# Kernel optimization log

Hardware: AMD Instinct MI355X
Metric: run time of the kernel (lower is better)

## Reference

```python
import jax, jax.numpy as jnp
import numpy as np

B = 262144
STATE_DIM = 12
ACTION_DIM = 1
MSG_DIM = 32
MAX_CHILDREN = 2
EPS = 1e-12  # F.normalize default eps


def _l2norm(x):
    n = jnp.sqrt(jnp.sum(x * x, axis=-1, keepdims=True))
    return x / jnp.maximum(n, EPS)


def setup_inputs() -> dict:
    key = jax.random.key(0)
    ks = jax.random.split(key, 16)

    def lin(kw, kb, out_d, in_d):
        lim = 1.0 / np.sqrt(in_d)
        w = jax.random.uniform(kw, (out_d, in_d), jnp.float32, -lim, lim)
        b = jax.random.uniform(kb, (out_d,), jnp.float32, -lim, lim)
        return w, b

    state = jax.random.normal(ks[0], (B, STATE_DIM), jnp.float32)
    action = jax.random.normal(ks[1], (B, ACTION_DIM), jnp.float32)

    # ModelUp (sNet): fc1, fc2, fc3
    up_w1, up_b1 = lin(ks[2], ks[3], 64, STATE_DIM + ACTION_DIM)
    up_w2, up_b2 = lin(ks[4], ks[5], 64, 64 + MSG_DIM * MAX_CHILDREN)
    up_w3, up_b3 = lin(ks[6], ks[7], MSG_DIM, 64)

    # ModelDownAction.model = MLPBase(msg_dim + action_dim + msg_dim, msg_dim)
    dyn_w1, dyn_b1 = lin(ks[8], ks[9], 400, MSG_DIM + ACTION_DIM + MSG_DIM)
    dyn_w2, dyn_b2 = lin(ks[10], ks[11], 300, 400)
    dyn_w3, dyn_b3 = lin(ks[12], ks[13], MSG_DIM, 300)

    return dict(state=state, action=action,
                up_w1=up_w1, up_b1=up_b1, up_w2=up_w2, up_b2=up_b2,
                up_w3=up_w3, up_b3=up_b3,
                dyn_w1=dyn_w1, dyn_b1=dyn_b1, dyn_w2=dyn_w2, dyn_b2=dyn_b2,
                dyn_w3=dyn_w3, dyn_b3=dyn_b3)


def reference(state, action,
              up_w1, up_b1, up_w2, up_b2, up_w3, up_b3,
              dyn_w1, dyn_b1, dyn_w2, dyn_b2, dyn_w3, dyn_b3):
    # num_limbs == 1, parents = [-1], td = bu = True, disable_fold = True
    x = state                              # (B, state_dim)
    u = action                             # (B, 1)

    # ---- bottom_up_transmission(0): ModelUp with all-zero child messages ----
    m_children = jnp.zeros((B, MSG_DIM * MAX_CHILDREN), x.dtype)
    xu = jnp.concatenate([x, u], axis=-1)
    xu = _l2norm(xu @ up_w1.T + up_b1)                       # (B, 64)
    xum = jnp.tanh(jnp.concatenate([xu, m_children], axis=-1))
    xum = jnp.tanh(xum @ up_w2.T + up_b2)                    # (B, 64)
    msg_up = _l2norm(xum @ up_w3.T + up_b3)                  # (B, msg_dim)

    # ---- top_down_transmission(0): ModelDownAction, state := msg_up ----
    # parent_msg = zeros, self_children_idx = 0 -> msg_in = zeros slice
    msg_in = jnp.zeros((B, MSG_DIM), x.dtype)
    xum2 = jnp.concatenate([msg_up, u, msg_in], axis=-1)     # (B, 2*msg_dim+1)
    h = jax.nn.relu(xum2 @ dyn_w1.T + dyn_b1)                # (B, 400)
    h = jax.nn.relu(h @ dyn_w2.T + dyn_b2)                   # (B, 300)
    delta = h @ dyn_w3.T + dyn_b3                            # (B, msg_dim)

    # stack over num_limbs=1 then squeeze -> (B, msg_dim)
    return delta
```

## Files before the change

### kernel.cpp

```cpp
#include <hip/hip_runtime.h>
#include <stdint.h>

typedef short s16x8 __attribute__((ext_vector_type(8)));
typedef float f32x16 __attribute__((ext_vector_type(16)));
typedef unsigned int u32;
typedef unsigned int u32x2 __attribute__((ext_vector_type(2)));

#define NFRAG 336
#define WS_USHORTS (NFRAG*512)
#define PANEL_BYTES 28672
#define LDS_BYTES (2*PANEL_BYTES)

#define MFMA(a,b,c) __builtin_amdgcn_mfma_f32_32x32x16_bf16((a),(b),(c),0,0,0)

__device__ __forceinline__ unsigned short f2bf(float f){
  u32 x = __builtin_bit_cast(u32, f);
  x += 0x7fffu + ((x >> 16) & 1u);
  return (unsigned short)(x >> 16);
}

__device__ __forceinline__ float bfhi(float b){
  return __builtin_bit_cast(float, (u32)f2bf(b) << 16);
}

__device__ __forceinline__ u32 pkbf(float a, float b){
  u32 r;
  asm("v_cvt_pk_bf16_f32 %0, %1, %2" : "=v"(r) : "v"(a), "v"(b));
  return r;
}

__device__ __forceinline__ float fast_tanh(float x){
  float ax = fabsf(x);
  float e = __expf(-2.0f * ax);
  float r = (1.0f - e) * __builtin_amdgcn_rcpf(1.0f + e);
  return x < 0.0f ? -r : r;
}

__device__ __forceinline__ float halfsum(float s){
  return s + __shfl_xor(s, 32);
}

__device__ __forceinline__ void tile2frags(const f32x16 v, s16x8& f0, s16x8& f1){
  u32 w00 = pkbf(v[0],  v[1]),  w01 = pkbf(v[2],  v[3]);
  u32 w10 = pkbf(v[4],  v[5]),  w11 = pkbf(v[6],  v[7]);
  u32 w20 = pkbf(v[8],  v[9]),  w21 = pkbf(v[10], v[11]);
  u32 w30 = pkbf(v[12], v[13]), w31 = pkbf(v[14], v[15]);
  u32x2 p0 = __builtin_amdgcn_permlane32_swap(w00, w10, false, false);
  u32x2 p1 = __builtin_amdgcn_permlane32_swap(w01, w11, false, false);
  u32x2 p2 = __builtin_amdgcn_permlane32_swap(w20, w30, false, false);
  u32x2 p3 = __builtin_amdgcn_permlane32_swap(w21, w31, false, false);
  int4 r0, r1;
  r0.x = (int)p0[0]; r0.y = (int)p1[0]; r0.z = (int)p0[1]; r0.w = (int)p1[1];
  r1.x = (int)p2[0]; r1.y = (int)p3[0]; r1.z = (int)p2[1]; r1.w = (int)p3[1];
  f0 = __builtin_bit_cast(s16x8, r0);
  f1 = __builtin_bit_cast(s16x8, r1);
}

__global__ void wconv_kernel(const float* __restrict__ uw1, const float* __restrict__ ub1,
                             const float* __restrict__ uw2, const float* __restrict__ ub2,
                             const float* __restrict__ uw3, const float* __restrict__ ub3,
                             const float* __restrict__ dw1, const float* __restrict__ db1,
                             const float* __restrict__ dw2, const float* __restrict__ db2,
                             const float* __restrict__ dw3, const float* __restrict__ db3,
                             unsigned short* __restrict__ wp)
{
  int i = blockIdx.x*256 + threadIdx.x;
  if (i >= WS_USHORTS) return;
  int f    = i >> 9;
  int lane = (i >> 3) & 63;
  int j    = i & 7;
  int row  = lane & 31;
  int k8   = (lane >> 5)*8 + j;
  float v = 0.0f;
  if (f < 2){
    int feat = f*32 + row; int k = k8;
    if (k < 13) v = uw1[feat*13 + k];
    else if (k == 13) v = ub1[feat];
    else if (k == 14) v = ub1[feat] - bfhi(ub1[feat]);
  } else if (f < 12){
    int t = f - 2; int kt = t >> 1, nt = t & 1;
    int feat = nt*32 + row; int k = kt*16 + k8;
    if (k < 64) v = uw2[feat*128 + k];
    else if (k == 64) v = ub2[feat];
    else if (k == 65) v = ub2[feat] - bfhi(ub2[feat]);
  } else if (f < 17){
    int kt = f - 12; int feat = row; int k = kt*16 + k8;
    if (k < 64) v = uw3[feat*64 + k];
    else if (k == 64) v = ub3[feat];
    else if (k == 65) v = ub3[feat] - bfhi(ub3[feat]);
  } else if (f < 56){
    int t = f - 17; int nt = t/3, kt = t%3;
    int feat = nt*32 + row; int k = kt*16 + k8;
    if (feat < 400){
      if (k < 33) v = dw1[feat*65 + k];
      else if (k == 33) v = db1[feat];
      else if (k == 34) v = db1[feat] - bfhi(db1[feat]);
    } else if ((feat == 400 || feat == 401) && k == 33) v = 1.0f;
  } else {
    int t = f - 56; int n = t/56; int r = t%56;
    if (r < 52){
      int kf = r >> 1, nt = r & 1;
      int feat = n*64 + nt*32 + row; int k = kf*16 + k8;
      if (feat < 300){
        if (k < 400) v = dw2[feat*400 + k];
        else if (k == 400) v = db2[feat];
        else if (k == 401) v = db2[feat] - bfhi(db2[feat]);
      } else if ((feat == 300 || feat == 301) && k == 400) v = 1.0f;
    } else {
      int kt = n*4 + (r - 52); int feat = row; int k = kt*16 + k8;
      if (k < 300) v = dw3[feat*300 + k];
      else if (k == 300) v = db3[feat];
      else if (k == 301) v = db3[feat] - bfhi(db3[feat]);
    }
  }
  wp[i] = f2bf(v);
}

__device__ __forceinline__ s16x8 frag_at(const char* P, int idx, int ln){
  return *(const s16x8*)(P + idx*1024 + ln*16);
}

__device__ __forceinline__ void stage_chunk(const unsigned short* wp, char* dst,
                                            int fbase, int nf, int tid){
  const char* src = (const char*)wp + (size_t)fbase*1024;
  int nbytes = nf*1024;
  #pragma unroll
  for (int j = 0; j < 7; ++j){
    int off = j*4096 + tid*16;
    if (off < nbytes)
      __builtin_amdgcn_global_load_lds(
        (const __attribute__((address_space(1))) unsigned int*)(src + off),
        (__attribute__((address_space(3))) unsigned int*)(dst + off), 16, 0, 0);
  }
}

__global__ __launch_bounds__(256, 2) void fused_kernel(
    const float* __restrict__ state, const float* __restrict__ action,
    const unsigned short* __restrict__ wp, float* __restrict__ out)
{
  __shared__ __align__(1024) char sm[LDS_BYTES];
  char* B0 = sm;
  char* B1 = sm + PANEL_BYTES;

  const int tid = threadIdx.x;
  const int ln  = tid & 63;
  const int wid = tid >> 6;
  const int c   = ln & 31;
  const int h   = ln >> 5;
  const int rowb = blockIdx.x*128 + wid*32;

  const float* xr = state + (size_t)(rowb + c)*12;
  float u = action[rowb + c];
  float4 xa, xb;
  if (h == 0){
    xa = *(const float4*)xr;
    xb = *(const float4*)(xr + 4);
  } else {
    xa = *(const float4*)(xr + 8);
    xb = float4{u, 1.0f, 1.0f, 0.0f};
  }

  stage_chunk(wp, B0, 0, 17, tid);
  __syncthreads();
  stage_chunk(wp, B1, 17, 21, tid);

  int4 xw;
  xw.x = pkbf(xa.x, xa.y); xw.y = pkbf(xa.z, xa.w);
  xw.z = pkbf(xb.x, xb.y); xw.w = pkbf(xb.z, xb.w);
  s16x8 xfrag = __builtin_bit_cast(s16x8, xw);
  int4 ow = {0,0,0,0}; if (h == 0) ow.x = 0x3F803F80;
  s16x8 onef = __builtin_bit_cast(s16x8, ow);
  int4 mw = {0,0,0,0};
  if (h == 0){ mw.x = pkbf(u, 1.0f); mw.y = 0x3F80; }
  s16x8 mf2 = __builtin_bit_cast(s16x8, mw);

  s16x8 mf0, mf1;
  {
    s16x8 xf0, xf1, xf2, xf3, tf0, tf1, tf2, tf3;
    {
      f32x16 a0 = {}, a1 = {};
      a0 = MFMA(frag_at(B0, 0, ln), xfrag, a0);
      a1 = MFMA(frag_at(B0, 1, ln), xfrag, a1);
      float s = 0.f;
      #pragma unroll
      for (int r = 0; r < 16; ++r) s += a0[r]*a0[r] + a1[r]*a1[r];
      s = halfsum(s);
      float inv = __builtin_amdgcn_rsqf(fmaxf(s, 1e-24f));
      #pragma unroll
      for (int r = 0; r < 16; ++r){
        a0[r] = fast_tanh(a0[r]*inv);
        a1[r] = fast_tanh(a1[r]*inv);
      }
      tile2frags(a0, xf0, xf1);
      tile2frags(a1, xf2, xf3);
    }
    {
      f32x16 a0 = {}, a1 = {};
      __builtin_amdgcn_s_setprio(1);
      a0 = MFMA(frag_at(B0, 2, ln), xf0, a0);  a1 = MFMA(frag_at(B0, 3, ln), xf0, a1);
      a0 = MFMA(frag_at(B0, 4, ln), xf1, a0);  a1 = MFMA(frag_at(B0, 5, ln), xf1, a1);
      a0 = MFMA(frag_at(B0, 6, ln), xf2, a0);  a1 = MFMA(frag_at(B0, 7, ln), xf2, a1);
      a0 = MFMA(frag_at(B0, 8, ln), xf3, a0);  a1 = MFMA(frag_at(B0, 9, ln), xf3, a1);
      a0 = MFMA(frag_at(B0,10, ln), onef, a0); a1 = MFMA(frag_at(B0,11, ln), onef, a1);
      __builtin_amdgcn_s_setprio(0);
      #pragma unroll
      for (int r = 0; r < 16; ++r){
        a0[r] = fast_tanh(a0[r]);
        a1[r] = fast_tanh(a1[r]);
      }
      tile2frags(a0, tf0, tf1);
      tile2frags(a1, tf2, tf3);
    }
    {
      f32x16 m = {};
      __builtin_amdgcn_s_setprio(1);
      m = MFMA(frag_at(B0,12, ln), tf0, m);
      m = MFMA(frag_at(B0,13, ln), tf1, m);
      m = MFMA(frag_at(B0,14, ln), tf2, m);
      m = MFMA(frag_at(B0,15, ln), tf3, m);
      m = MFMA(frag_at(B0,16, ln), onef, m);
      __builtin_amdgcn_s_setprio(0);
      float s = 0.f;
      #pragma unroll
      for (int r = 0; r < 16; ++r) s += m[r]*m[r];
      s = halfsum(s);
      float inv = __builtin_amdgcn_rsqf(fmaxf(s, 1e-24f));
      #pragma unroll
      for (int r = 0; r < 16; ++r) m[r] *= inv;
      tile2frags(m, mf0, mf1);
    }
  }

  s16x8 h1f[26];

  __syncthreads();
  stage_chunk(wp, B0, 38, 18, tid);
  #pragma unroll
  for (int nt = 0; nt < 7; ++nt){
    f32x16 a = {};
    __builtin_amdgcn_s_setprio(1);
    a = MFMA(frag_at(B1, nt*3+0, ln), mf0, a);
    a = MFMA(frag_at(B1, nt*3+1, ln), mf1, a);
    a = MFMA(frag_at(B1, nt*3+2, ln), mf2, a);
    __builtin_amdgcn_s_setprio(0);
    #pragma unroll
    for (int r = 0; r < 16; ++r) a[r] = fmaxf(a[r], 0.f);
    tile2frags(a, h1f[2*nt], h1f[2*nt+1]);
  }

  __syncthreads();
  stage_chunk(wp, B1, 56, 28, tid);
  #pragma unroll
  for (int nt = 0; nt < 6; ++nt){
    f32x16 a = {};
    __builtin_amdgcn_s_setprio(1);
    a = MFMA(frag_at(B0, nt*3+0, ln), mf0, a);
    a = MFMA(frag_at(B0, nt*3+1, ln), mf1, a);
    a = MFMA(frag_at(B0, nt*3+2, ln), mf2, a);
    __builtin_amdgcn_s_setprio(0);
    #pragma unroll
    for (int r = 0; r < 16; ++r) a[r] = fmaxf(a[r], 0.f);
    tile2frags(a, h1f[14 + 2*nt], h1f[14 + 2*nt+1]);
  }

  f32x16 acc3 = {};
  #pragma unroll 1
  for (int n = 0; n < 5; ++n){
    f32x16 d2a0 = {}, d2a1 = {};

    __syncthreads();
    stage_chunk(wp, B0, 84 + 56*n, 28, tid);
    __builtin_amdgcn_s_setprio(1);
    #pragma unroll
    for (int kfl = 0; kfl < 14; ++kfl){
      s16x8 hb = h1f[kfl];
      d2a0 = MFMA(frag_at(B1, kfl*2+0, ln), hb, d2a0);
      d2a1 = MFMA(frag_at(B1, kfl*2+1, ln), hb, d2a1);
    }
    __builtin_amdgcn_s_setprio(0);

    __syncthreads();
    if (n < 4) stage_chunk(wp, B1, 56 + 56*(n+1), 28, tid);
    __builtin_amdgcn_s_setprio(1);
    #pragma unroll
    for (int kfl = 0; kfl < 12; ++kfl){
      s16x8 hb = h1f[14 + kfl];
      d2a0 = MFMA(frag_at(B0, kfl*2+0, ln), hb, d2a0);
      d2a1 = MFMA(frag_at(B0, kfl*2+1, ln), hb, d2a1);
    }
    __builtin_amdgcn_s_setprio(0);
    #pragma unroll
    for (int r = 0; r < 16; ++r){
      d2a0[r] = fmaxf(d2a0[r], 0.f);
      d2a1[r] = fmaxf(d2a1[r], 0.f);
    }
    s16x8 c0, c1, c2, c3;
    tile2frags(d2a0, c0, c1);
    tile2frags(d2a1, c2, c3);
    __builtin_amdgcn_s_setprio(1);
    acc3 = MFMA(frag_at(B0, 24, ln), c0, acc3);
    acc3 = MFMA(frag_at(B0, 25, ln), c1, acc3);
    acc3 = MFMA(frag_at(B0, 26, ln), c2, acc3);
    acc3 = MFMA(frag_at(B0, 27, ln), c3, acc3);
    __builtin_amdgcn_s_setprio(0);
  }

  float* op = out + (size_t)(rowb + c)*32;
  #pragma unroll
  for (int p = 0; p < 4; ++p){
    float4 v4 = {acc3[4*p+0], acc3[4*p+1], acc3[4*p+2], acc3[4*p+3]};
    *(float4*)(op + p*8 + h*4) = v4;
  }
}

extern "C" void kernel_launch(void* const* d_in, const int* in_sizes, int n_in,
                              void* d_out, int out_size, void* d_ws, size_t ws_size,
                              hipStream_t stream)
{
  const float* state  = (const float*)d_in[0];
  const float* action = (const float*)d_in[1];
  const float* up_w1  = (const float*)d_in[2];
  const float* up_b1  = (const float*)d_in[3];
  const float* up_w2  = (const float*)d_in[4];
  const float* up_b2  = (const float*)d_in[5];
  const float* up_w3  = (const float*)d_in[6];
  const float* up_b3  = (const float*)d_in[7];
  const float* dyn_w1 = (const float*)d_in[8];
  const float* dyn_b1 = (const float*)d_in[9];
  const float* dyn_w2 = (const float*)d_in[10];
  const float* dyn_b2 = (const float*)d_in[11];
  const float* dyn_w3 = (const float*)d_in[12];
  const float* dyn_b3 = (const float*)d_in[13];
  unsigned short* wp = (unsigned short*)d_ws;

  hipLaunchKernelGGL(wconv_kernel, dim3((WS_USHORTS + 255)/256), dim3(256), 0, stream,
                     up_w1, up_b1, up_w2, up_b2, up_w3, up_b3,
                     dyn_w1, dyn_b1, dyn_w2, dyn_b2, dyn_w3, dyn_b3, wp);
  hipLaunchKernelGGL(fused_kernel, dim3(262144/128), dim3(256), 0, stream,
                     state, action, wp, (float*)d_out);
}
```

Measured before the change: 95.67 us.

## Stream weights in uniform 16-fragment panels with smaller 2-wave blocks

Replaces the irregular chunk staging (17/21/18/28-fragment chunks in two 28KB panels) with a uniform ring of 16KB panels, each holding 16 weight fragments, and addresses fragments by a global index. Panel loads are issued at fixed barrier points spread through the layer computations, so the double buffer advances at a steady rate. Blocks shrink from 4 waves/128 rows to 2 waves/64 rows, halving LDS per block so more blocks fit per CU. The cost is that each block stages the full weight set for half as many rows, doubling total global-to-LDS weight traffic, and there are more barriers.

```diff
diff --git a/kernel.cpp b/kernel.cpp
--- a/kernel.cpp
+++ b/kernel.cpp
@@ -8,7 +8,7 @@
 
 #define NFRAG 336
 #define WS_USHORTS (NFRAG*512)
-#define PANEL_BYTES 28672
+#define PANEL_BYTES 16384
 #define LDS_BYTES (2*PANEL_BYTES)
 
 #define MFMA(a,b,c) __builtin_amdgcn_mfma_f32_32x32x16_bf16((a),(b),(c),0,0,0)
@@ -116,38 +116,73 @@
   wp[i] = f2bf(v);
 }
 
-__device__ __forceinline__ s16x8 frag_at(const char* P, int idx, int ln){
-  return *(const s16x8*)(P + idx*1024 + ln*16);
-}
-
-__device__ __forceinline__ void stage_chunk(const unsigned short* wp, char* dst,
-                                            int fbase, int nf, int tid){
-  const char* src = (const char*)wp + (size_t)fbase*1024;
-  int nbytes = nf*1024;
+__device__ __forceinline__ s16x8 fragF(const char* sm, int f, int ln){
+  return *(const s16x8*)(sm + ((f >> 4) & 1)*PANEL_BYTES + (f & 15)*1024 + ln*16);
+}
+
+__device__ __forceinline__ void stage16(const unsigned short* wp, char* sm, int panel, int tid){
+  char* dst = sm + (panel & 1)*PANEL_BYTES;
+  const char* src = (const char*)wp + (size_t)panel*PANEL_BYTES;
   #pragma unroll
-  for (int j = 0; j < 7; ++j){
-    int off = j*4096 + tid*16;
-    if (off < nbytes)
-      __builtin_amdgcn_global_load_lds(
-        (const __attribute__((address_space(1))) unsigned int*)(src + off),
-        (__attribute__((address_space(3))) unsigned int*)(dst + off), 16, 0, 0);
-  }
-}
-
-__global__ __launch_bounds__(256, 2) void fused_kernel(
+  for (int j = 0; j < 8; ++j){
+    int off = j*2048 + tid*16;
+    __builtin_amdgcn_global_load_lds(
+      (const __attribute__((address_space(1))) unsigned int*)(src + off),
+      (__attribute__((address_space(3))) unsigned int*)(dst + off), 16, 0, 0);
+  }
+}
+
+#define BND(P) { __syncthreads(); if ((P) <= 20) stage16(wp, sm, (P), tid); }
+
+#define D1TRIPLE(f0_, oA, oB) { \
+  f32x16 a = {}; \
+  __builtin_amdgcn_s_setprio(1); \
+  a = MFMA(fragF(sm, (f0_)+0, ln), mf0, a); \
+  a = MFMA(fragF(sm, (f0_)+1, ln), mf1, a); \
+  a = MFMA(fragF(sm, (f0_)+2, ln), mf2, a); \
+  __builtin_amdgcn_s_setprio(0); \
+  _Pragma("unroll") \
+  for (int r = 0; r < 16; ++r) a[r] = fmaxf(a[r], 0.f); \
+  tile2frags(a, oA, oB); }
+
+#define D2RUN(fb, r0, r1) { \
+  __builtin_amdgcn_s_setprio(1); \
+  _Pragma("unroll") \
+  for (int r = (r0); r < (r1); ++r){ \
+    s16x8 hb = h1f[r>>1]; \
+    if (r & 1) d2a1 = MFMA(fragF(sm, (fb)+r, ln), hb, d2a1); \
+    else       d2a0 = MFMA(fragF(sm, (fb)+r, ln), hb, d2a0); \
+  } \
+  __builtin_amdgcn_s_setprio(0); }
+
+#define D2TAIL(fb) { \
+  _Pragma("unroll") \
+  for (int r = 0; r < 16; ++r){ \
+    d2a0[r] = fmaxf(d2a0[r], 0.f); \
+    d2a1[r] = fmaxf(d2a1[r], 0.f); \
+  } \
+  s16x8 c0, c1, c2, c3; \
+  tile2frags(d2a0, c0, c1); \
+  tile2frags(d2a1, c2, c3); \
+  __builtin_amdgcn_s_setprio(1); \
+  acc3 = MFMA(fragF(sm, (fb)+52, ln), c0, acc3); \
+  acc3 = MFMA(fragF(sm, (fb)+53, ln), c1, acc3); \
+  acc3 = MFMA(fragF(sm, (fb)+54, ln), c2, acc3); \
+  acc3 = MFMA(fragF(sm, (fb)+55, ln), c3, acc3); \
+  __builtin_amdgcn_s_setprio(0); }
+
+__global__ __launch_bounds__(128, 2) void fused_kernel(
     const float* __restrict__ state, const float* __restrict__ action,
     const unsigned short* __restrict__ wp, float* __restrict__ out)
 {
   __shared__ __align__(1024) char sm[LDS_BYTES];
-  char* B0 = sm;
-  char* B1 = sm + PANEL_BYTES;
 
   const int tid = threadIdx.x;
   const int ln  = tid & 63;
   const int wid = tid >> 6;
   const int c   = ln & 31;
   const int h   = ln >> 5;
-  const int rowb = blockIdx.x*128 + wid*32;
+  const int rowb = blockIdx.x*64 + wid*32;
 
   const float* xr = state + (size_t)(rowb + c)*12;
   float u = action[rowb + c];
@@ -160,9 +195,8 @@
     xb = float4{u, 1.0f, 1.0f, 0.0f};
   }
 
-  stage_chunk(wp, B0, 0, 17, tid);
-  __syncthreads();
-  stage_chunk(wp, B1, 17, 21, tid);
+  stage16(wp, sm, 0, tid);
+  BND(1)
 
   int4 xw;
   xw.x = pkbf(xa.x, xa.y); xw.y = pkbf(xa.z, xa.w);
@@ -179,8 +213,8 @@
     s16x8 xf0, xf1, xf2, xf3, tf0, tf1, tf2, tf3;
     {
       f32x16 a0 = {}, a1 = {};
-      a0 = MFMA(frag_at(B0, 0, ln), xfrag, a0);
-      a1 = MFMA(frag_at(B0, 1, ln), xfrag, a1);
+      a0 = MFMA(fragF(sm, 0, ln), xfrag, a0);
+      a1 = MFMA(fragF(sm, 1, ln), xfrag, a1);
       float s = 0.f;
       #pragma unroll
       for (int r = 0; r < 16; ++r) s += a0[r]*a0[r] + a1[r]*a1[r];
@@ -197,11 +231,11 @@
     {
       f32x16 a0 = {}, a1 = {};
       __builtin_amdgcn_s_setprio(1);
-      a0 = MFMA(frag_at(B0, 2, ln), xf0, a0);  a1 = MFMA(frag_at(B0, 3, ln), xf0, a1);
-      a0 = MFMA(frag_at(B0, 4, ln), xf1, a0);  a1 = MFMA(frag_at(B0, 5, ln), xf1, a1);
-      a0 = MFMA(frag_at(B0, 6, ln), xf2, a0);  a1 = MFMA(frag_at(B0, 7, ln), xf2, a1);
-      a0 = MFMA(frag_at(B0, 8, ln), xf3, a0);  a1 = MFMA(frag_at(B0, 9, ln), xf3, a1);
-      a0 = MFMA(frag_at(B0,10, ln), onef, a0); a1 = MFMA(frag_at(B0,11, ln), onef, a1);
+      a0 = MFMA(fragF(sm, 2, ln), xf0, a0);  a1 = MFMA(fragF(sm, 3, ln), xf0, a1);
+      a0 = MFMA(fragF(sm, 4, ln), xf1, a0);  a1 = MFMA(fragF(sm, 5, ln), xf1, a1);
+      a0 = MFMA(fragF(sm, 6, ln), xf2, a0);  a1 = MFMA(fragF(sm, 7, ln), xf2, a1);
+      a0 = MFMA(fragF(sm, 8, ln), xf3, a0);  a1 = MFMA(fragF(sm, 9, ln), xf3, a1);
+      a0 = MFMA(fragF(sm,10, ln), onef, a0); a1 = MFMA(fragF(sm,11, ln), onef, a1);
       __builtin_amdgcn_s_setprio(0);
       #pragma unroll
       for (int r = 0; r < 16; ++r){
@@ -214,11 +248,14 @@
     {
       f32x16 m = {};
       __builtin_amdgcn_s_setprio(1);
-      m = MFMA(frag_at(B0,12, ln), tf0, m);
-      m = MFMA(frag_at(B0,13, ln), tf1, m);
-      m = MFMA(frag_at(B0,14, ln), tf2, m);
-      m = MFMA(frag_at(B0,15, ln), tf3, m);
-      m = MFMA(frag_at(B0,16, ln), onef, m);
+      m = MFMA(fragF(sm,12, ln), tf0, m);
+      m = MFMA(fragF(sm,13, ln), tf1, m);
+      m = MFMA(fragF(sm,14, ln), tf2, m);
+      m = MFMA(fragF(sm,15, ln), tf3, m);
+      __builtin_amdgcn_s_setprio(0);
+      BND(2)
+      __builtin_amdgcn_s_setprio(1);
+      m = MFMA(fragF(sm,16, ln), onef, m);
       __builtin_amdgcn_s_setprio(0);
       float s = 0.f;
       #pragma unroll
@@ -232,77 +269,91 @@
   }
 
   s16x8 h1f[26];
-
-  __syncthreads();
-  stage_chunk(wp, B0, 38, 18, tid);
-  #pragma unroll
-  for (int nt = 0; nt < 7; ++nt){
+  D1TRIPLE(17, h1f[0],  h1f[1])
+  D1TRIPLE(20, h1f[2],  h1f[3])
+  D1TRIPLE(23, h1f[4],  h1f[5])
+  D1TRIPLE(26, h1f[6],  h1f[7])
+  D1TRIPLE(29, h1f[8],  h1f[9])
+  BND(3)
+  D1TRIPLE(32, h1f[10], h1f[11])
+  D1TRIPLE(35, h1f[12], h1f[13])
+  D1TRIPLE(38, h1f[14], h1f[15])
+  D1TRIPLE(41, h1f[16], h1f[17])
+  D1TRIPLE(44, h1f[18], h1f[19])
+  {
     f32x16 a = {};
     __builtin_amdgcn_s_setprio(1);
-    a = MFMA(frag_at(B1, nt*3+0, ln), mf0, a);
-    a = MFMA(frag_at(B1, nt*3+1, ln), mf1, a);
-    a = MFMA(frag_at(B1, nt*3+2, ln), mf2, a);
+    a = MFMA(fragF(sm, 47, ln), mf0, a);
+    __builtin_amdgcn_s_setprio(0);
+    BND(4)
+    __builtin_amdgcn_s_setprio(1);
+    a = MFMA(fragF(sm, 48, ln), mf1, a);
+    a = MFMA(fragF(sm, 49, ln), mf2, a);
     __builtin_amdgcn_s_setprio(0);
     #pragma unroll
     for (int r = 0; r < 16; ++r) a[r] = fmaxf(a[r], 0.f);
-    tile2frags(a, h1f[2*nt], h1f[2*nt+1]);
-  }
-
-  __syncthreads();
-  stage_chunk(wp, B1, 56, 28, tid);
-  #pragma unroll
-  for (int nt = 0; nt < 6; ++nt){
-    f32x16 a = {};
-    __builtin_amdgcn_s_setprio(1);
-    a = MFMA(frag_at(B0, nt*3+0, ln), mf0, a);
-    a = MFMA(frag_at(B0, nt*3+1, ln), mf1, a);
-    a = MFMA(frag_at(B0, nt*3+2, ln), mf2, a);
-    __builtin_amdgcn_s_setprio(0);
-    #pragma unroll
-    for (int r = 0; r < 16; ++r) a[r] = fmaxf(a[r], 0.f);
-    tile2frags(a, h1f[14 + 2*nt], h1f[14 + 2*nt+1]);
-  }
+    tile2frags(a, h1f[20], h1f[21]);
+  }
+  D1TRIPLE(50, h1f[22], h1f[23])
+  D1TRIPLE(53, h1f[24], h1f[25])
 
   f32x16 acc3 = {};
-  #pragma unroll 1
-  for (int n = 0; n < 5; ++n){
-    f32x16 d2a0 = {}, d2a1 = {};
-
-    __syncthreads();
-    stage_chunk(wp, B0, 84 + 56*n, 28, tid);
-    __builtin_amdgcn_s_setprio(1);
-    #pragma unroll
-    for (int kfl = 0; kfl < 14; ++kfl){
-      s16x8 hb = h1f[kfl];
-      d2a0 = MFMA(frag_at(B1, kfl*2+0, ln), hb, d2a0);
-      d2a1 = MFMA(frag_at(B1, kfl*2+1, ln), hb, d2a1);
-    }
-    __builtin_amdgcn_s_setprio(0);
-
-    __syncthreads();
-    if (n < 4) stage_chunk(wp, B1, 56 + 56*(n+1), 28, tid);
-    __builtin_amdgcn_s_setprio(1);
-    #pragma unroll
-    for (int kfl = 0; kfl < 12; ++kfl){
-      s16x8 hb = h1f[14 + kfl];
-      d2a0 = MFMA(frag_at(B0, kfl*2+0, ln), hb, d2a0);
-      d2a1 = MFMA(frag_at(B0, kfl*2+1, ln), hb, d2a1);
-    }
-    __builtin_amdgcn_s_setprio(0);
-    #pragma unroll
-    for (int r = 0; r < 16; ++r){
-      d2a0[r] = fmaxf(d2a0[r], 0.f);
-      d2a1[r] = fmaxf(d2a1[r], 0.f);
-    }
-    s16x8 c0, c1, c2, c3;
-    tile2frags(d2a0, c0, c1);
-    tile2frags(d2a1, c2, c3);
-    __builtin_amdgcn_s_setprio(1);
-    acc3 = MFMA(frag_at(B0, 24, ln), c0, acc3);
-    acc3 = MFMA(frag_at(B0, 25, ln), c1, acc3);
-    acc3 = MFMA(frag_at(B0, 26, ln), c2, acc3);
-    acc3 = MFMA(frag_at(B0, 27, ln), c3, acc3);
-    __builtin_amdgcn_s_setprio(0);
+  {
+    f32x16 d2a0 = {}, d2a1 = {};
+    D2RUN(56, 0, 8)
+    BND(5)
+    D2RUN(56, 8, 24)
+    BND(6)
+    D2RUN(56, 24, 40)
+    BND(7)
+    D2RUN(56, 40, 52)
+    D2TAIL(56)
+  }
+  {
+    f32x16 d2a0 = {}, d2a1 = {};
+    BND(8)
+    D2RUN(112, 0, 16)
+    BND(9)
+    D2RUN(112, 16, 32)
+    BND(10)
+    D2RUN(112, 32, 48)
+    BND(11)
+    D2RUN(112, 48, 52)
+    D2TAIL(112)
+  }
+  {
+    f32x16 d2a0 = {}, d2a1 = {};
+    D2RUN(168, 0, 8)
+    BND(12)
+    D2RUN(168, 8, 24)
+    BND(13)
+    D2RUN(168, 24, 40)
+    BND(14)
+    D2RUN(168, 40, 52)
+    D2TAIL(168)
+  }
+  {
+    f32x16 d2a0 = {}, d2a1 = {};
+    BND(15)
+    D2RUN(224, 0, 16)
+    BND(16)
+    D2RUN(224, 16, 32)
+    BND(17)
+    D2RUN(224, 32, 48)
+    BND(18)
+    D2RUN(224, 48, 52)
+    D2TAIL(224)
+  }
+  {
+    f32x16 d2a0 = {}, d2a1 = {};
+    D2RUN(280, 0, 8)
+    BND(19)
+    D2RUN(280, 8, 24)
+    BND(20)
+    D2RUN(280, 24, 40)
+    BND(21)
+    D2RUN(280, 40, 52)
+    D2TAIL(280)
   }
 
   float* op = out + (size_t)(rowb + c)*32;
@@ -336,6 +387,6 @@
   hipLaunchKernelGGL(wconv_kernel, dim3((WS_USHORTS + 255)/256), dim3(256), 0, stream,
                      up_w1, up_b1, up_w2, up_b2, up_w3, up_b3,
                      dyn_w1, dyn_b1, dyn_w2, dyn_b2, dyn_w3, dyn_b3, wp);
-  hipLaunchKernelGGL(fused_kernel, dim3(262144/128), dim3(256), 0, stream,
+  hipLaunchKernelGGL(fused_kernel, dim3(262144/64), dim3(128), 0, stream,
                      state, action, wp, (float*)d_out);
 }
```

After: 104.6 us. +9.4%, slower.
